# Performance work log

Measured on AMD Instinct MI355X. Metric: run time of the kernel, lower is better.

## Reference

```python
import jax, jax.numpy as jnp
import numpy as np

N_NODES = 100_000
N_EDGES = 1_600_000
N_FEAT = 64
HIDDEN = 64
BIOPRINT = 2048
N_GRAPHS = 1024


def setup_inputs() -> dict:
    key = jax.random.key(0)
    ks = jax.random.split(key, 12)
    x = jax.random.normal(ks[0], (N_NODES, N_FEAT), jnp.float32)
    edge_index = jax.random.randint(ks[1], (2, N_EDGES), 0, N_NODES, dtype=jnp.int64)
    batch = jnp.sort(jax.random.randint(ks[2], (N_NODES,), 0, N_GRAPHS, dtype=jnp.int64))
    def lin(k, fan_in, fan_out):
        s = 1.0 / np.sqrt(fan_in)
        return jax.random.uniform(k, (fan_in, fan_out), jnp.float32, -s, s)
    W1 = lin(ks[3], N_FEAT, HIDDEN)
    b1 = jnp.zeros((HIDDEN,), jnp.float32)
    W2 = lin(ks[4], HIDDEN, HIDDEN)
    b2 = jnp.zeros((HIDDEN,), jnp.float32)
    W3 = lin(ks[5], HIDDEN, HIDDEN)
    b3 = jnp.zeros((HIDDEN,), jnp.float32)
    Wd = lin(ks[6], HIDDEN, BIOPRINT)
    bd = jax.random.uniform(ks[7], (BIOPRINT,), jnp.float32, -1.0 / np.sqrt(HIDDEN), 1.0 / np.sqrt(HIDDEN))
    return {"x": x, "edge_index": edge_index, "batch": batch,
            "W1": W1, "b1": b1, "W2": W2, "b2": b2, "W3": W3, "b3": b3,
            "Wd": Wd, "bd": bd}


def reference(x, edge_index, batch, W1, b1, W2, b2, W3, b3, Wd, bd):
    n = x.shape[0]
    src, dst = edge_index[0], edge_index[1]
    # GCN symmetric normalization with self-loops: deg = in-degree + 1
    ones_e = jnp.ones(src.shape[0], x.dtype)
    deg = jax.ops.segment_sum(ones_e, dst, num_segments=n) + 1.0
    dinv = jax.lax.rsqrt(deg)  # deg >= 1 always
    self_norm = (dinv * dinv)[:, None]
    edge_norm = (dinv[src] * dinv[dst])[:, None]

    def gcn_conv(h, W, b):
        hw = h @ W  # [N, out]
        agg = jax.ops.segment_sum(hw[src] * edge_norm, dst, num_segments=n)
        return agg + hw * self_norm + b  # self-loop handled analytically

    h = jax.nn.relu(gcn_conv(x, W1, b1))
    h = jax.nn.relu(gcn_conv(h, W2, b2))
    h = gcn_conv(h, W3, b3)

    # global_mean_pool over graph ids
    cnt = jax.ops.segment_sum(jnp.ones(n, x.dtype), batch, num_segments=N_GRAPHS)
    pooled = jax.ops.segment_sum(h, batch, num_segments=N_GRAPHS) / jnp.maximum(cnt, 1.0)[:, None]

    # dropout(p=0.5) is identity in eval mode
    logits = pooled @ Wd + bd
    probs = jax.nn.softmax(logits, axis=-1)
    return (probs >= 0.5).astype(x.dtype)
```

## Files before the change

### kernel.cpp

```cpp
#include <hip/hip_runtime.h>
#include <hip/hip_fp16.h>
#include <math.h>

#define N_NODES   100000
#define N_EDGES   1600000
#define N_FEAT    64
#define HIDDEN    64
#define BIOPRINT  2048
#define N_GRAPHS  1024

#define SENTINEL  N_NODES
#define COL_CAP   (N_EDGES + 8 * N_NODES)

#define SCAN_BLK  1024
#define N_SCAN_BLOCKS ((N_NODES + SCAN_BLK - 1) / SCAN_BLK)
#define N_E4 (N_EDGES / 4)
#define FILL_BLOCKS ((N_E4 + 255) / 256)
#define MM_ROWS   32
#define MM_GRID32 (N_NODES / MM_ROWS)
#define DEG_BLOCKS ((N_E4 + 255) / 256)

__device__ __forceinline__ __half2 shx_h2(__half2 v, int m) {
    int x = __shfl_xor(*(int*)&v, m);
    return *(__half2*)&x;
}

__device__ __forceinline__ void stage_w_perm(const float* __restrict__ W, float* sW, int t) {
    const float4* W4 = (const float4*)W;
    for (int i = t; i < 1024; i += 256) {
        float4 w = W4[i];
        int k = i >> 4;
        int c4 = (i & 15) * 4;
        int base = (k >> 2) * 256 + (k & 3);
        sW[base + (c4 + 0) * 4] = w.x;
        sW[base + (c4 + 1) * 4] = w.y;
        sW[base + (c4 + 2) * 4] = w.z;
        sW[base + (c4 + 3) * 4] = w.w;
    }
}


__global__ __launch_bounds__(256) void k_deg(const int* __restrict__ dst,
                                             int* __restrict__ deg,
                                             int* __restrict__ rank) {
    int tid = blockIdx.x * blockDim.x + threadIdx.x;
    if (tid >= N_E4) return;
    int4 d4 = ((const int4*)dst)[tid];
    int4 r4;
    r4.x = atomicAdd(&deg[d4.x], 1);
    r4.y = atomicAdd(&deg[d4.y], 1);
    r4.z = atomicAdd(&deg[d4.z], 1);
    r4.w = atomicAdd(&deg[d4.w], 1);
    ((int4*)rank)[tid] = r4;
}


__global__ __launch_bounds__(SCAN_BLK) void k_scan1(
        const int* __restrict__ deg, int* __restrict__ incl,
        int* __restrict__ bsum, float* __restrict__ dinv, int n) {
    __shared__ int tmp[SCAN_BLK];
    int t = threadIdx.x;
    int i = blockIdx.x * SCAN_BLK + t;
    int v = (i < n) ? deg[i] : 0;
    if (i < n) dinv[i] = rsqrtf((float)v + 1.0f);
    int vp = (v + 7) & ~7;
    tmp[t] = vp;
    __syncthreads();
    for (int off = 1; off < SCAN_BLK; off <<= 1) {
        int u = (t >= off) ? tmp[t - off] : 0;
        __syncthreads();
        tmp[t] += u;
        __syncthreads();
    }
    if (i < n) incl[i] = tmp[t];
    if (t == SCAN_BLK - 1) bsum[blockIdx.x] = tmp[t];
}

__global__ __launch_bounds__(SCAN_BLK) void k_scan3(
        int* __restrict__ rowptr, const int* __restrict__ deg,
        const int* __restrict__ bsum, int* __restrict__ col,
        const int* __restrict__ batch, int* __restrict__ gstart, int n) {
    int t = threadIdx.x;
    int bid = blockIdx.x;
    if (bid >= N_SCAN_BLOCKS) {
        int g = (bid - N_SCAN_BLOCKS) * SCAN_BLK + t;
        if (g > N_GRAPHS) return;
        if (g == N_GRAPHS) { gstart[g] = N_NODES; return; }
        int lo = 0, hi = N_NODES;
        while (lo < hi) { int mid = (lo + hi) >> 1; if (batch[mid] < g) lo = mid + 1; else hi = mid; }
        gstart[g] = lo;
        return;
    }
    __shared__ int sb[128];
    if (t < 128) sb[t] = (t < N_SCAN_BLOCKS) ? bsum[t] : 0;
    __syncthreads();
    for (int off = 1; off < 128; off <<= 1) {
        int u = (t >= off && t < 128) ? sb[t - off] : 0;
        __syncthreads();
        if (t < 128) sb[t] += u;
        __syncthreads();
    }
    int base = (bid == 0) ? 0 : sb[bid - 1];
    int i = bid * SCAN_BLK + t;
    if (i < n) {
        int v = deg[i];
        int vp = (v + 7) & ~7;
        int ex = rowptr[i] - vp + base;
        rowptr[i] = ex;
        for (int j = v; j < vp; ++j) col[ex + j] = SENTINEL;
    }
    if (bid == 0 && t == 0) rowptr[n] = sb[N_SCAN_BLOCKS - 1];
}

__global__ __launch_bounds__(256) void k_fillmm(
        const int* __restrict__ src, const int* __restrict__ dst,
        const int* __restrict__ rank, const int* __restrict__ rowptr,
        int* __restrict__ col,
        const float* __restrict__ h, const float* __restrict__ W,
        const float* __restrict__ dinv, __half* __restrict__ hw) {
    int bid = blockIdx.x;
    if (bid < FILL_BLOCKS) {
        int tid = bid * 256 + threadIdx.x;
        if (tid < N_E4) {
            int4 d4 = ((const int4*)dst)[tid];
            int4 r4 = ((const int4*)rank)[tid];
            int4 s4 = ((const int4*)src)[tid];
            col[rowptr[d4.x] + r4.x] = s4.x;
            col[rowptr[d4.y] + r4.y] = s4.y;
            col[rowptr[d4.z] + r4.z] = s4.z;
            col[rowptr[d4.w] + r4.w] = s4.w;
        }
        return;
    }
    __shared__ float sW[64 * 64];
    __shared__ float sA[MM_ROWS * 64];
    int t = threadIdx.x;
    stage_w_perm(W, sW, t);
    int row0 = (bid - FILL_BLOCKS) * MM_ROWS;
    ((float4*)sA)[t]       = ((const float4*)h)[row0 * 16 + t];
    ((float4*)sA)[t + 256] = ((const float4*)h)[row0 * 16 + t + 256];
    __syncthreads();
    int wave = t >> 6, lane = t & 63;
    const float4* sWp = (const float4*)sW;
    float sum[8] = {0.f, 0.f, 0.f, 0.f, 0.f, 0.f, 0.f, 0.f};
#pragma unroll
    for (int k4 = 0; k4 < 16; ++k4) {
        float4 w4 = sWp[k4 * 64 + lane];
#pragma unroll
        for (int hh = 0; hh < 8; ++hh) {
            float4 a4 = ((const float4*)&sA[(wave * 8 + hh) * 64])[k4];
            sum[hh] = fmaf(a4.x, w4.x, sum[hh]);
            sum[hh] = fmaf(a4.y, w4.y, sum[hh]);
            sum[hh] = fmaf(a4.z, w4.z, sum[hh]);
            sum[hh] = fmaf(a4.w, w4.w, sum[hh]);
        }
    }
#pragma unroll
    for (int hh = 0; hh < 8; ++hh) {
        int row = row0 + wave * 8 + hh;
        hw[(size_t)row * 64 + lane] = __float2half_rn(sum[hh] * dinv[row]);
    }
}

__device__ __forceinline__ void gather2x4(
        const int* __restrict__ col, const uint4* __restrict__ hv,
        int rs, int re, int slot, int sub, float f[8]) {
    __half2 a0 = __float2half2_rn(0.f), a1 = a0, a2 = a0, a3 = a0;
    __half2 c0 = a0, c1 = a0, c2 = a0, c3 = a0;
    for (int e = rs; e < re; e += 8) {
        int s0 = __builtin_nontemporal_load(&col[e + slot]);
        int s1 = __builtin_nontemporal_load(&col[e + 2 + slot]);
        int s2 = __builtin_nontemporal_load(&col[e + 4 + slot]);
        int s3 = __builtin_nontemporal_load(&col[e + 6 + slot]);
        uint4 u0 = hv[(size_t)s0 * 8 + sub];
        uint4 u1 = hv[(size_t)s1 * 8 + sub];
        uint4 u2 = hv[(size_t)s2 * 8 + sub];
        uint4 u3 = hv[(size_t)s3 * 8 + sub];
        a0 = __hadd2(a0, *(__half2*)&u0.x); a1 = __hadd2(a1, *(__half2*)&u0.y);
        a2 = __hadd2(a2, *(__half2*)&u0.z); a3 = __hadd2(a3, *(__half2*)&u0.w);
        c0 = __hadd2(c0, *(__half2*)&u1.x); c1 = __hadd2(c1, *(__half2*)&u1.y);
        c2 = __hadd2(c2, *(__half2*)&u1.z); c3 = __hadd2(c3, *(__half2*)&u1.w);
        a0 = __hadd2(a0, *(__half2*)&u2.x); a1 = __hadd2(a1, *(__half2*)&u2.y);
        a2 = __hadd2(a2, *(__half2*)&u2.z); a3 = __hadd2(a3, *(__half2*)&u2.w);
        c0 = __hadd2(c0, *(__half2*)&u3.x); c1 = __hadd2(c1, *(__half2*)&u3.y);
        c2 = __hadd2(c2, *(__half2*)&u3.z); c3 = __hadd2(c3, *(__half2*)&u3.w);
    }
    a0 = __hadd2(a0, c0); a1 = __hadd2(a1, c1);
    a2 = __hadd2(a2, c2); a3 = __hadd2(a3, c3);
    a0 = __hadd2(a0, shx_h2(a0, 8));
    a1 = __hadd2(a1, shx_h2(a1, 8));
    a2 = __hadd2(a2, shx_h2(a2, 8));
    a3 = __hadd2(a3, shx_h2(a3, 8));
    float2 f0 = __half22float2(a0), f1 = __half22float2(a1);
    float2 f2 = __half22float2(a2), f3 = __half22float2(a3);
    f[0] = f0.x; f[1] = f0.y; f[2] = f1.x; f[3] = f1.y;
    f[4] = f2.x; f[5] = f2.y; f[6] = f3.x; f[7] = f3.y;
}

__global__ __launch_bounds__(256) void k_gmm(
        const int* __restrict__ rowptr, const int* __restrict__ col,
        const float* __restrict__ dinv, const float* __restrict__ b,
        const __half* __restrict__ hw_in, const float* __restrict__ W,
        __half* __restrict__ hw_out) {
    __shared__ float sW[64 * 64];
    __shared__ float sA[16 * 64];
    int t = threadIdx.x;
    stage_w_perm(W, sW, t);
    __syncthreads();

    int wave = t >> 6, lane = t & 63;
    int quarter = lane >> 4, slot = (lane >> 3) & 1, sub = lane & 7;
    int i0 = blockIdx.x * 16 + wave * 4;
    int i = i0 + quarter;
    float di = dinv[i];
    int rs = rowptr[i], re = rowptr[i + 1];
    const uint4* hv = (const uint4*)hw_in;

    float f[8];
    gather2x4(col, hv, rs, re, slot, sub, f);

    uint4 us = hv[(size_t)i * 8 + sub];
    float2 s0 = __half22float2(*(__half2*)&us.x);
    float2 s1 = __half22float2(*(__half2*)&us.y);
    float2 s2 = __half22float2(*(__half2*)&us.z);
    float2 s3 = __half22float2(*(__half2*)&us.w);
    float sf[8] = {s0.x, s0.y, s1.x, s1.y, s2.x, s2.y, s3.x, s3.y};
    float4 ba = ((const float4*)b)[sub * 2];
    float4 bb = ((const float4*)b)[sub * 2 + 1];
    float bf[8] = {ba.x, ba.y, ba.z, ba.w, bb.x, bb.y, bb.z, bb.w};
    if (slot == 0) {
        float r[8];
#pragma unroll
        for (int k = 0; k < 8; ++k) r[k] = fmaxf(fmaf(di, f[k] + sf[k], bf[k]), 0.f);
        *(float4*)&sA[(wave * 4 + quarter) * 64 + sub * 8]     = make_float4(r[0], r[1], r[2], r[3]);
        *(float4*)&sA[(wave * 4 + quarter) * 64 + sub * 8 + 4] = make_float4(r[4], r[5], r[6], r[7]);
    }

    const float4* sWp = (const float4*)sW;
    float sum[4] = {0.f, 0.f, 0.f, 0.f};
#pragma unroll
    for (int k4 = 0; k4 < 16; ++k4) {
        float4 w4 = sWp[k4 * 64 + lane];
#pragma unroll
        for (int hh = 0; hh < 4; ++hh) {
            float4 a4 = ((const float4*)&sA[(wave * 4 + hh) * 64])[k4];
            sum[hh] = fmaf(a4.x, w4.x, sum[hh]);
            sum[hh] = fmaf(a4.y, w4.y, sum[hh]);
            sum[hh] = fmaf(a4.z, w4.z, sum[hh]);
            sum[hh] = fmaf(a4.w, w4.w, sum[hh]);
        }
    }
#pragma unroll
    for (int hh = 0; hh < 4; ++hh)
        hw_out[(size_t)(i0 + hh) * 64 + lane] = __float2half_rn(sum[hh] * dinv[i0 + hh]);
}

__global__ __launch_bounds__(256) void k_gather3(
        const int* __restrict__ rowptr, const int* __restrict__ col,
        const float* __restrict__ dinv, const float* __restrict__ b,
        const __half* __restrict__ hw_in, __half* __restrict__ conv) {
    int t = threadIdx.x;
    int wave = t >> 6, lane = t & 63;
    int quarter = lane >> 4, slot = (lane >> 3) & 1, sub = lane & 7;
    int i = blockIdx.x * 16 + wave * 4 + quarter;
    float di = dinv[i];
    int rs = rowptr[i], re = rowptr[i + 1];
    const uint4* hv = (const uint4*)hw_in;

    float f[8];
    gather2x4(col, hv, rs, re, slot, sub, f);

    if (slot == 0) {
        uint4 us = hv[(size_t)i * 8 + sub];
        float2 s0 = __half22float2(*(__half2*)&us.x);
        float2 s1 = __half22float2(*(__half2*)&us.y);
        float2 s2 = __half22float2(*(__half2*)&us.z);
        float2 s3 = __half22float2(*(__half2*)&us.w);
        float sf[8] = {s0.x, s0.y, s1.x, s1.y, s2.x, s2.y, s3.x, s3.y};
        float4 ba = ((const float4*)b)[sub * 2];
        float4 bb = ((const float4*)b)[sub * 2 + 1];
        float bf[8] = {ba.x, ba.y, ba.z, ba.w, bb.x, bb.y, bb.z, bb.w};
        uint4 o;
        __half2* oh = (__half2*)&o;
#pragma unroll
        for (int c = 0; c < 4; ++c) {
            float r0 = fmaf(di, f[2 * c] + sf[2 * c], bf[2 * c]);
            float r1 = fmaf(di, f[2 * c + 1] + sf[2 * c + 1], bf[2 * c + 1]);
            oh[c] = __halves2half2(__float2half_rn(r0), __float2half_rn(r1));
        }
        ((uint4*)conv)[(size_t)i * 8 + sub] = o;
    }
}

__global__ __launch_bounds__(256) void k_dense(
        const __half* __restrict__ conv, const int* __restrict__ gstart,
        const float* __restrict__ Wd, const float* __restrict__ bd,
        float* __restrict__ out) {
    __shared__ float sred[4][64];
    __shared__ float sp[64];
    __shared__ float rmax[4];
    __shared__ float rsum[4];
    int t = threadIdx.x;
    int wave = t >> 6, lane = t & 63;
    int g = blockIdx.x;
    int n0 = gstart[g], n1 = gstart[g + 1];

    int fp = lane & 31;
    int par = lane >> 5;
    const __half2* conv2 = (const __half2*)conv;
    float2 acc2 = make_float2(0.f, 0.f);
    for (int i = n0 + wave * 2 + par; i < n1; i += 8) {
        float2 f = __half22float2(conv2[(size_t)i * 32 + fp]);
        acc2.x += f.x; acc2.y += f.y;
    }
    acc2.x += __shfl_xor(acc2.x, 32);
    acc2.y += __shfl_xor(acc2.y, 32);
    if (lane < 32) { sred[wave][2 * fp] = acc2.x; sred[wave][2 * fp + 1] = acc2.y; }
    __syncthreads();
    if (t < 64) {
        int n = n1 - n0;
        float s = sred[0][t] + sred[1][t] + sred[2][t] + sred[3][t];
        sp[t] = (n > 0) ? s / (float)n : 0.f;
    }
    __syncthreads();

    float acc[8];
#pragma unroll
    for (int r = 0; r < 8; ++r) acc[r] = bd[r * 256 + t];
    for (int k = 0; k < 64; ++k) {
        float h = sp[k];
#pragma unroll
        for (int r = 0; r < 8; ++r)
            acc[r] = fmaf(h, Wd[k * BIOPRINT + r * 256 + t], acc[r]);
    }

    float m = acc[0];
#pragma unroll
    for (int r = 1; r < 8; ++r) m = fmaxf(m, acc[r]);
#pragma unroll
    for (int off = 32; off > 0; off >>= 1) m = fmaxf(m, __shfl_xor(m, off));
    if (lane == 0) rmax[wave] = m;
    __syncthreads();
    m = fmaxf(fmaxf(rmax[0], rmax[1]), fmaxf(rmax[2], rmax[3]));

    float s = 0.f;
#pragma unroll
    for (int r = 0; r < 8; ++r) { acc[r] = expf(acc[r] - m); s += acc[r]; }
#pragma unroll
    for (int off = 32; off > 0; off >>= 1) s += __shfl_xor(s, off);
    if (lane == 0) rsum[wave] = s;
    __syncthreads();
    s = rsum[0] + rsum[1] + rsum[2] + rsum[3];

#pragma unroll
    for (int r = 0; r < 8; ++r) {
        float p = acc[r] / s;
        out[(size_t)g * BIOPRINT + r * 256 + t] = (p >= 0.5f) ? 1.0f : 0.0f;
    }
}


extern "C" void kernel_launch(void* const* d_in, const int* in_sizes, int n_in,
                              void* d_out, int out_size, void* d_ws, size_t ws_size,
                              hipStream_t stream) {
    const float* x     = (const float*)d_in[0];
    const int*   ei    = (const int*)d_in[1];
    const int*   batch = (const int*)d_in[2];
    const float* W1 = (const float*)d_in[3];
    const float* b1 = (const float*)d_in[4];
    const float* W2 = (const float*)d_in[5];
    const float* b2 = (const float*)d_in[6];
    const float* W3 = (const float*)d_in[7];
    const float* b3 = (const float*)d_in[8];
    const float* Wd = (const float*)d_in[9];
    const float* bd = (const float*)d_in[10];
    float* out = (float*)d_out;

    const int* src = ei;
    const int* dst = ei + N_EDGES;

    char* ws = (char*)d_ws;
    size_t off = 0;
    auto alloc = [&](size_t bytes) {
        void* p = ws + off;
        off += (bytes + 255) & ~(size_t)255;
        return p;
    };
    int*    deg    = (int*)alloc(N_NODES * sizeof(int));
    float*  dinv   = (float*)alloc(N_NODES * sizeof(float));
    int*    rowptr = (int*)alloc((N_NODES + 1) * sizeof(int));
    int*    bsum   = (int*)alloc(128 * sizeof(int));
    int*    rank   = (int*)alloc((size_t)N_EDGES * sizeof(int));
    int*    gstart = (int*)alloc((N_GRAPHS + 1) * sizeof(int));
    int*    col    = (int*)alloc((size_t)COL_CAP * sizeof(int));
    __half* bufA   = (__half*)alloc((size_t)(N_NODES + 1) * HIDDEN * sizeof(__half));
    __half* bufB   = (__half*)alloc((size_t)(N_NODES + 1) * HIDDEN * sizeof(__half));
    __half* conv   = (__half*)alloc((size_t)N_NODES * HIDDEN * sizeof(__half));

    hipMemsetAsync(deg, 0, N_NODES * sizeof(int), stream);
    hipMemsetAsync(bufA + (size_t)N_NODES * HIDDEN, 0, HIDDEN * sizeof(__half), stream);
    hipMemsetAsync(bufB + (size_t)N_NODES * HIDDEN, 0, HIDDEN * sizeof(__half), stream);

    k_deg<<<DEG_BLOCKS, 256, 0, stream>>>(dst, deg, rank);
    k_scan1<<<N_SCAN_BLOCKS, SCAN_BLK, 0, stream>>>(deg, rowptr, bsum, dinv, N_NODES);
    k_scan3<<<N_SCAN_BLOCKS + 2, SCAN_BLK, 0, stream>>>(rowptr, deg, bsum, col,
                                                        batch, gstart, N_NODES);
    k_fillmm<<<FILL_BLOCKS + MM_GRID32, 256, 0, stream>>>(src, dst, rank, rowptr, col,
                                                          x, W1, dinv, bufA);

    const int g16_grid = N_NODES / 16;
    k_gmm<<<g16_grid, 256, 0, stream>>>(rowptr, col, dinv, b1, bufA, W2, bufB);
    k_gmm<<<g16_grid, 256, 0, stream>>>(rowptr, col, dinv, b2, bufB, W3, bufA);
    k_gather3<<<g16_grid, 256, 0, stream>>>(rowptr, col, dinv, b3, bufA, conv);
    k_dense<<<N_GRAPHS, 256, 0, stream>>>(conv, gstart, Wd, bd, out);
}
```

Before: 353.9 us.

## Replace CSR construction with fixed-stride ELL adjacency filled directly by atomics

Drops the degree pass, the two-stage prefix scan, the rank array and the separate CSR fill. Each edge now takes its slot from the atomic degree counter and writes straight into a 64-slot-per-node ELL column array. The first matmul no longer waits for degrees: it writes unscaled features, and a new prep kernel applies the rsqrt degree scaling, pads the rows with sentinel entries and computes graph starts. This removes several launches and the scan serialisation. In exchange it uses a larger column array and an extra pass over the features, and it assumes no node has more than 56 in-edges; above that, slots wrap or padded rows spill into the next node's row.

```diff
diff --git a/kernel.cpp b/kernel.cpp
--- a/kernel.cpp
+++ b/kernel.cpp
@@ -10,15 +10,12 @@
 #define N_GRAPHS  1024
 
 #define SENTINEL  N_NODES
-#define COL_CAP   (N_EDGES + 8 * N_NODES)
-
-#define SCAN_BLK  1024
-#define N_SCAN_BLOCKS ((N_NODES + SCAN_BLK - 1) / SCAN_BLK)
+#define ELL_STRIDE 64
+
 #define N_E4 (N_EDGES / 4)
-#define FILL_BLOCKS ((N_E4 + 255) / 256)
-#define MM_ROWS   32
-#define MM_GRID32 (N_NODES / MM_ROWS)
 #define DEG_BLOCKS ((N_E4 + 255) / 256)
+#define MM1_BLOCKS (N_NODES / 32)
+#define GS_BLOCKS  5
 
 __device__ __forceinline__ __half2 shx_h2(__half2 v, int m) {
     int x = __shfl_xor(*(int*)&v, m);
@@ -39,106 +36,32 @@
     }
 }
 
-
-__global__ __launch_bounds__(256) void k_deg(const int* __restrict__ dst,
-                                             int* __restrict__ deg,
-                                             int* __restrict__ rank) {
-    int tid = blockIdx.x * blockDim.x + threadIdx.x;
-    if (tid >= N_E4) return;
-    int4 d4 = ((const int4*)dst)[tid];
-    int4 r4;
-    r4.x = atomicAdd(&deg[d4.x], 1);
-    r4.y = atomicAdd(&deg[d4.y], 1);
-    r4.z = atomicAdd(&deg[d4.z], 1);
-    r4.w = atomicAdd(&deg[d4.w], 1);
-    ((int4*)rank)[tid] = r4;
-}
-
-
-__global__ __launch_bounds__(SCAN_BLK) void k_scan1(
-        const int* __restrict__ deg, int* __restrict__ incl,
-        int* __restrict__ bsum, float* __restrict__ dinv, int n) {
-    __shared__ int tmp[SCAN_BLK];
+__global__ __launch_bounds__(256) void k_degmm(
+        const int* __restrict__ src, const int* __restrict__ dst,
+        int* __restrict__ deg, int* __restrict__ colELL,
+        const float* __restrict__ x, const float* __restrict__ W,
+        __half* __restrict__ hw) {
+    int bid = blockIdx.x;
     int t = threadIdx.x;
-    int i = blockIdx.x * SCAN_BLK + t;
-    int v = (i < n) ? deg[i] : 0;
-    if (i < n) dinv[i] = rsqrtf((float)v + 1.0f);
-    int vp = (v + 7) & ~7;
-    tmp[t] = vp;
-    __syncthreads();
-    for (int off = 1; off < SCAN_BLK; off <<= 1) {
-        int u = (t >= off) ? tmp[t - off] : 0;
-        __syncthreads();
-        tmp[t] += u;
-        __syncthreads();
-    }
-    if (i < n) incl[i] = tmp[t];
-    if (t == SCAN_BLK - 1) bsum[blockIdx.x] = tmp[t];
-}
-
-__global__ __launch_bounds__(SCAN_BLK) void k_scan3(
-        int* __restrict__ rowptr, const int* __restrict__ deg,
-        const int* __restrict__ bsum, int* __restrict__ col,
-        const int* __restrict__ batch, int* __restrict__ gstart, int n) {
-    int t = threadIdx.x;
-    int bid = blockIdx.x;
-    if (bid >= N_SCAN_BLOCKS) {
-        int g = (bid - N_SCAN_BLOCKS) * SCAN_BLK + t;
-        if (g > N_GRAPHS) return;
-        if (g == N_GRAPHS) { gstart[g] = N_NODES; return; }
-        int lo = 0, hi = N_NODES;
-        while (lo < hi) { int mid = (lo + hi) >> 1; if (batch[mid] < g) lo = mid + 1; else hi = mid; }
-        gstart[g] = lo;
-        return;
-    }
-    __shared__ int sb[128];
-    if (t < 128) sb[t] = (t < N_SCAN_BLOCKS) ? bsum[t] : 0;
-    __syncthreads();
-    for (int off = 1; off < 128; off <<= 1) {
-        int u = (t >= off && t < 128) ? sb[t - off] : 0;
-        __syncthreads();
-        if (t < 128) sb[t] += u;
-        __syncthreads();
-    }
-    int base = (bid == 0) ? 0 : sb[bid - 1];
-    int i = bid * SCAN_BLK + t;
-    if (i < n) {
-        int v = deg[i];
-        int vp = (v + 7) & ~7;
-        int ex = rowptr[i] - vp + base;
-        rowptr[i] = ex;
-        for (int j = v; j < vp; ++j) col[ex + j] = SENTINEL;
-    }
-    if (bid == 0 && t == 0) rowptr[n] = sb[N_SCAN_BLOCKS - 1];
-}
-
-__global__ __launch_bounds__(256) void k_fillmm(
-        const int* __restrict__ src, const int* __restrict__ dst,
-        const int* __restrict__ rank, const int* __restrict__ rowptr,
-        int* __restrict__ col,
-        const float* __restrict__ h, const float* __restrict__ W,
-        const float* __restrict__ dinv, __half* __restrict__ hw) {
-    int bid = blockIdx.x;
-    if (bid < FILL_BLOCKS) {
-        int tid = bid * 256 + threadIdx.x;
+    if (bid < DEG_BLOCKS) {
+        int tid = bid * 256 + t;
         if (tid < N_E4) {
             int4 d4 = ((const int4*)dst)[tid];
-            int4 r4 = ((const int4*)rank)[tid];
             int4 s4 = ((const int4*)src)[tid];
-            col[rowptr[d4.x] + r4.x] = s4.x;
-            col[rowptr[d4.y] + r4.y] = s4.y;
-            col[rowptr[d4.z] + r4.z] = s4.z;
-            col[rowptr[d4.w] + r4.w] = s4.w;
+            int r;
+            r = atomicAdd(&deg[d4.x], 1); colELL[d4.x * ELL_STRIDE + (r & 63)] = s4.x;
+            r = atomicAdd(&deg[d4.y], 1); colELL[d4.y * ELL_STRIDE + (r & 63)] = s4.y;
+            r = atomicAdd(&deg[d4.z], 1); colELL[d4.z * ELL_STRIDE + (r & 63)] = s4.z;
+            r = atomicAdd(&deg[d4.w], 1); colELL[d4.w * ELL_STRIDE + (r & 63)] = s4.w;
         }
         return;
     }
     __shared__ float sW[64 * 64];
-    __shared__ float sA[MM_ROWS * 64];
-    int t = threadIdx.x;
+    __shared__ float sA[32 * 64];
     stage_w_perm(W, sW, t);
-    int row0 = (bid - FILL_BLOCKS) * MM_ROWS;
-    ((float4*)sA)[t]       = ((const float4*)h)[row0 * 16 + t];
-    ((float4*)sA)[t + 256] = ((const float4*)h)[row0 * 16 + t + 256];
+    int row0 = (bid - DEG_BLOCKS) * 32;
+    ((float4*)sA)[t]       = ((const float4*)x)[row0 * 16 + t];
+    ((float4*)sA)[t + 256] = ((const float4*)x)[row0 * 16 + t + 256];
     __syncthreads();
     int wave = t >> 6, lane = t & 63;
     const float4* sWp = (const float4*)sW;
@@ -158,8 +81,43 @@
 #pragma unroll
     for (int hh = 0; hh < 8; ++hh) {
         int row = row0 + wave * 8 + hh;
-        hw[(size_t)row * 64 + lane] = __float2half_rn(sum[hh] * dinv[row]);
-    }
+        hw[(size_t)row * 64 + lane] = __float2half_rn(sum[hh]);
+    }
+}
+
+__global__ __launch_bounds__(256) void k_prep(
+        const int* __restrict__ deg, float* __restrict__ dinv,
+        int* __restrict__ colELL, __half* __restrict__ hw,
+        const int* __restrict__ batch, int* __restrict__ gstart) {
+    int bid = blockIdx.x, t = threadIdx.x;
+    if (bid < MM1_BLOCKS) {
+        int row0 = bid * 32;
+        int row = row0 + (t >> 3);
+        float di = rsqrtf((float)deg[row] + 1.0f);
+        uint4* p = (uint4*)hw;
+        uint4 v = p[(size_t)row * 8 + (t & 7)];
+        __half2* h2 = (__half2*)&v;
+#pragma unroll
+        for (int c = 0; c < 4; ++c) {
+            float2 f = __half22float2(h2[c]);
+            h2[c] = __halves2half2(__float2half_rn(f.x * di), __float2half_rn(f.y * di));
+        }
+        p[(size_t)row * 8 + (t & 7)] = v;
+        if ((t & 7) == 0) dinv[row] = di;
+        if (t < 32) {
+            int r2 = row0 + t;
+            int dv = deg[r2];
+            int vp = (dv + 7) & ~7;
+            for (int j = dv; j < vp; ++j) colELL[r2 * ELL_STRIDE + j] = SENTINEL;
+        }
+        return;
+    }
+    int g = (bid - MM1_BLOCKS) * 256 + t;
+    if (g > N_GRAPHS) return;
+    if (g == N_GRAPHS) { gstart[g] = N_NODES; return; }
+    int lo = 0, hi = N_NODES;
+    while (lo < hi) { int mid = (lo + hi) >> 1; if (batch[mid] < g) lo = mid + 1; else hi = mid; }
+    gstart[g] = lo;
 }
 
 __device__ __forceinline__ void gather2x4(
@@ -198,7 +156,7 @@
 }
 
 __global__ __launch_bounds__(256) void k_gmm(
-        const int* __restrict__ rowptr, const int* __restrict__ col,
+        const int* __restrict__ deg, const int* __restrict__ col,
         const float* __restrict__ dinv, const float* __restrict__ b,
         const __half* __restrict__ hw_in, const float* __restrict__ W,
         __half* __restrict__ hw_out) {
@@ -213,7 +171,8 @@
     int i0 = blockIdx.x * 16 + wave * 4;
     int i = i0 + quarter;
     float di = dinv[i];
-    int rs = rowptr[i], re = rowptr[i + 1];
+    int rs = i * ELL_STRIDE;
+    int re = rs + ((deg[i] + 7) & ~7);
     const uint4* hv = (const uint4*)hw_in;
 
     float f[8];
@@ -256,7 +215,7 @@
 }
 
 __global__ __launch_bounds__(256) void k_gather3(
-        const int* __restrict__ rowptr, const int* __restrict__ col,
+        const int* __restrict__ deg, const int* __restrict__ col,
         const float* __restrict__ dinv, const float* __restrict__ b,
         const __half* __restrict__ hw_in, __half* __restrict__ conv) {
     int t = threadIdx.x;
@@ -264,7 +223,8 @@
     int quarter = lane >> 4, slot = (lane >> 3) & 1, sub = lane & 7;
     int i = blockIdx.x * 16 + wave * 4 + quarter;
     float di = dinv[i];
-    int rs = rowptr[i], re = rowptr[i + 1];
+    int rs = i * ELL_STRIDE;
+    int re = rs + ((deg[i] + 7) & ~7);
     const uint4* hv = (const uint4*)hw_in;
 
     float f[8];
@@ -388,11 +348,8 @@
     };
     int*    deg    = (int*)alloc(N_NODES * sizeof(int));
     float*  dinv   = (float*)alloc(N_NODES * sizeof(float));
-    int*    rowptr = (int*)alloc((N_NODES + 1) * sizeof(int));
-    int*    bsum   = (int*)alloc(128 * sizeof(int));
-    int*    rank   = (int*)alloc((size_t)N_EDGES * sizeof(int));
     int*    gstart = (int*)alloc((N_GRAPHS + 1) * sizeof(int));
-    int*    col    = (int*)alloc((size_t)COL_CAP * sizeof(int));
+    int*    colELL = (int*)alloc((size_t)N_NODES * ELL_STRIDE * sizeof(int));
     __half* bufA   = (__half*)alloc((size_t)(N_NODES + 1) * HIDDEN * sizeof(__half));
     __half* bufB   = (__half*)alloc((size_t)(N_NODES + 1) * HIDDEN * sizeof(__half));
     __half* conv   = (__half*)alloc((size_t)N_NODES * HIDDEN * sizeof(__half));
@@ -401,16 +358,14 @@
     hipMemsetAsync(bufA + (size_t)N_NODES * HIDDEN, 0, HIDDEN * sizeof(__half), stream);
     hipMemsetAsync(bufB + (size_t)N_NODES * HIDDEN, 0, HIDDEN * sizeof(__half), stream);
 
-    k_deg<<<DEG_BLOCKS, 256, 0, stream>>>(dst, deg, rank);
-    k_scan1<<<N_SCAN_BLOCKS, SCAN_BLK, 0, stream>>>(deg, rowptr, bsum, dinv, N_NODES);
-    k_scan3<<<N_SCAN_BLOCKS + 2, SCAN_BLK, 0, stream>>>(rowptr, deg, bsum, col,
-                                                        batch, gstart, N_NODES);
-    k_fillmm<<<FILL_BLOCKS + MM_GRID32, 256, 0, stream>>>(src, dst, rank, rowptr, col,
-                                                          x, W1, dinv, bufA);
+    k_degmm<<<DEG_BLOCKS + MM1_BLOCKS, 256, 0, stream>>>(src, dst, deg, colELL,
+                                                         x, W1, bufA);
+    k_prep<<<MM1_BLOCKS + GS_BLOCKS, 256, 0, stream>>>(deg, dinv, colELL, bufA,
+                                                       batch, gstart);
 
     const int g16_grid = N_NODES / 16;
-    k_gmm<<<g16_grid, 256, 0, stream>>>(rowptr, col, dinv, b1, bufA, W2, bufB);
-    k_gmm<<<g16_grid, 256, 0, stream>>>(rowptr, col, dinv, b2, bufB, W3, bufA);
-    k_gather3<<<g16_grid, 256, 0, stream>>>(rowptr, col, dinv, b3, bufA, conv);
+    k_gmm<<<g16_grid, 256, 0, stream>>>(deg, colELL, dinv, b1, bufA, W2, bufB);
+    k_gmm<<<g16_grid, 256, 0, stream>>>(deg, colELL, dinv, b2, bufB, W3, bufA);
+    k_gather3<<<g16_grid, 256, 0, stream>>>(deg, colELL, dinv, b3, bufA, conv);
     k_dense<<<N_GRAPHS, 256, 0, stream>>>(conv, gstart, Wd, bd, out);
 }
```

Result: slower. 390.0 us (+10.2%).
